# Performance work log

Hardware: AMD Instinct MI355X
Metric: run time of the kernel (lower is better)

The kernel has to match this reference:

```python
import jax, jax.numpy as jnp
import numpy as np

NUM_EMBEDDINGS = 8192
EMBEDDING_DIM = 256
COMMITMENT_COST = 0.25


def setup_inputs() -> dict:
    key = jax.random.key(0)
    k1, k2 = jax.random.split(key)
    z = jax.random.normal(k1, (32, EMBEDDING_DIM, 32, 32), dtype=jnp.float32)
    embedding = jax.random.normal(k2, (EMBEDDING_DIM, NUM_EMBEDDINGS), dtype=jnp.float32)
    return {"z": z, "embedding": embedding}


def reference(z, embedding):
    # z: [B, D, H, W]; embedding: [D, K]
    B, D, H, W = z.shape
    z_perm = jnp.transpose(z, (0, 2, 3, 1))          # [B, H, W, D]
    flat_z = z_perm.reshape(-1, D)                    # [N, D]
    # squared euclidean distances: ||z||^2 - 2 z.e + ||e||^2  -> [N, K]
    distances = (
        jnp.sum(flat_z * flat_z, axis=1, keepdims=True)
        - 2.0 * (flat_z @ embedding)
        + jnp.sum(embedding * embedding, axis=0, keepdims=True)
    )
    encoding_indices = jnp.argmin(distances, axis=1)  # [N]
    # gather codebook rows (same math as one-hot @ embedding.T)
    quantized = jnp.take(embedding.T, encoding_indices, axis=0)  # [N, D]
    quantized = quantized.reshape(z_perm.shape)       # [B, H, W, D]
    quantized = jnp.transpose(quantized, (0, 3, 1, 2))  # [B, D, H, W]

    e_latent_loss = jnp.mean((jax.lax.stop_gradient(quantized) - z) ** 2)
    q_latent_loss = jnp.mean((quantized - jax.lax.stop_gradient(z)) ** 2)
    loss = q_latent_loss + COMMITMENT_COST * e_latent_loss

    # straight-through estimator
    quantized_st = z + jax.lax.stop_gradient(quantized - z)
    return quantized_st, loss
```

## Files before the change

### kernel.cpp

```cpp
#include <hip/hip_runtime.h>

typedef unsigned int u32;
typedef unsigned short u16;
typedef __attribute__((ext_vector_type(8))) short bf16x8;
typedef __attribute__((ext_vector_type(4))) float f32x4;

#define KN 8192
#define DD 256
#define HW 1024
#define NP 32768
#define SPLITS 2
#define KSPLIT 4096
#define BROW 256
#define BCOL 256
#define NTILES (KSPLIT / BCOL)

__device__ __forceinline__ u16 rne_bf16(float x) {
    u32 u = __float_as_uint(x);
    return (u16)((u + 0x7FFF + ((u >> 16) & 1)) >> 16);
}

__device__ __forceinline__ void glds16(const void* g, void* ldsbase) {
    __builtin_amdgcn_global_load_lds((const __attribute__((address_space(1))) u32*)g,
                                     (__attribute__((address_space(3))) u32*)ldsbase, 16, 0, 0);
}

__global__ void prep_kernel(const float* __restrict__ e, const float* __restrict__ z,
                            u16* __restrict__ eT, float* __restrict__ eTf,
                            float* __restrict__ e2f, u16* __restrict__ A) {
    const int t = threadIdx.x;
    const int bid = blockIdx.x;
    if (bid < 32) {
        int k = bid * 256 + t;
        float acc = 0.f;
#pragma unroll 8
        for (int d = 0; d < DD; ++d) {
            float v = e[(size_t)d * KN + k];
            acc = fmaf(v, v, acc);
        }
        e2f[k] = acc;
    } else if (bid < 544) {
        __shared__ float tt[64][65];
        const int b2 = bid - 32;
        const int kt = b2 & 127;
        const int dt = b2 >> 7;
        const float* ep = e + (size_t)(dt * 64) * KN + kt * 64;
        {
            int k = t & 63, d0 = t >> 6;
#pragma unroll
            for (int j = 0; j < 16; ++j) tt[d0 + j * 4][k] = ep[(size_t)(d0 + j * 4) * KN + k];
        }
        __syncthreads();
        int k = t >> 2, c0 = (t & 3) * 16;
        u16 hi[16];
        float fv[16];
#pragma unroll
        for (int j = 0; j < 16; ++j) {
            float v = tt[c0 + j][k];
            fv[j] = v;
            hi[j] = rne_bf16(v);
        }
        u16* rowp = eT + (size_t)(kt * 64 + k) * 256 + dt * 64 + c0;
        *(uint4*)(rowp) = *(uint4*)(hi);
        *(uint4*)(rowp + 8) = *(uint4*)(hi + 8);
        float* rowpf = eTf + (size_t)(kt * 64 + k) * 256 + dt * 64 + c0;
#pragma unroll
        for (int j = 0; j < 4; ++j) *(float4*)(rowpf + j * 4) = *(float4*)(fv + j * 4);
    } else {
        __shared__ float tt[64][65];
        const int b3 = bid - 544;
        const int pt = b3 & 15;
        const int dt = (b3 >> 4) & 3;
        const int b  = b3 >> 6;
        const float* zp = z + (size_t)b * (DD * HW) + (size_t)(dt * 64) * HW + pt * 64;
        {
            int p = t & 63, d0 = t >> 6;
#pragma unroll
            for (int j = 0; j < 16; ++j) tt[d0 + j * 4][p] = zp[(size_t)(d0 + j * 4) * HW + p];
        }
        __syncthreads();
        int p = t >> 2, c0 = (t & 3) * 16;
        int n = b * HW + pt * 64 + p;
        u16 hi[16];
#pragma unroll
        for (int j = 0; j < 16; ++j) hi[j] = rne_bf16(tt[c0 + j][p]);
        u16* rowp = A + (size_t)n * 256 + dt * 64 + c0;
        *(uint4*)(rowp) = *(uint4*)(hi);
        *(uint4*)(rowp + 8) = *(uint4*)(hi + 8);
    }
}


#define STAGE_A(kit)                                                              \
    do {                                                                          \
        const u16* as_ = asrc + (kit) * 32;                                       \
        glds16(as_,             &Ast[(kit) * 8192 + w * 512]);                    \
        glds16(as_ + 128 * 256, &Ast[(kit) * 8192 + (8 + w) * 512]);              \
    } while (0)

#define STAGE_B(eoff, buf)                                                        \
    do {                                                                          \
        const u16* bs_ = bsrc0 + (eoff);                                          \
        glds16(bs_,             &Bst[buf][w * 512]);                              \
        glds16(bs_ + 128 * 256, &Bst[buf][(8 + w) * 512]);                        \
    } while (0)

#define COMPUTE_KIT(kit, first)                                                   \
    do {                                                                          \
        bf16x8 af[4], bfr[8];                                                     \
        const u16* bq_ = &Bst[(kit) & 1][0];                                      \
        _Pragma("unroll")                                                         \
        for (int mi = 0; mi < 4; ++mi)                                            \
            af[mi] = *(const bf16x8*)&Ast[(kit) * 8192 + aoff + mi * 512];        \
        _Pragma("unroll")                                                         \
        for (int ni = 0; ni < 8; ++ni)                                            \
            bfr[ni] = *(const bf16x8*)&bq_[boff + ni * 512];                      \
        __builtin_amdgcn_s_setprio(1);                                            \
        _Pragma("unroll")                                                         \
        for (int mi = 0; mi < 4; ++mi)                                            \
            _Pragma("unroll")                                                     \
            for (int ni = 0; ni < 8; ++ni)                                        \
                acc[mi][ni] = __builtin_amdgcn_mfma_f32_16x16x32_bf16(            \
                    af[mi], bfr[ni], (first) ? zacc : acc[mi][ni], 0, 0, 0);      \
        __builtin_amdgcn_s_setprio(0);                                            \
    } while (0)

__launch_bounds__(512, 2)
__global__ void argmin_mfma_kernel(const u16* __restrict__ A,
                                   const u16* __restrict__ eT,
                                   const float* __restrict__ e2f,
                                   int* __restrict__ keys) {
    __shared__ __align__(16) u16 Ast[8 * 8192];
    __shared__ __align__(16) u16 Bst[2][8192];

    const int t = threadIdx.x;
    const int w = t >> 6;
    const int l = t & 63;
    const int wm = w & 3;
    const int wn = w >> 2;
    const int fr = l & 15;
    const int g  = l >> 4;

    const int split = blockIdx.x & 1;
    const int pxt   = blockIdx.x >> 1;
    const int px0 = pxt * BROW;
    const int kb0 = split * KSPLIT;

    const int srow = l >> 2;
    const int ssw  = ((l & 3) ^ ((l >> 2) & 3)) * 8;
    const u16* asrc  = A  + (size_t)(px0 + w * 16 + srow) * 256 + ssw;
    const u16* bsrc0 = eT + (size_t)(w * 16 + srow) * 256 + ssw;

    const int fsw  = (g ^ (fr & 3)) * 8;
    const int aoff = (wm * 64 + fr) * 32 + fsw;
    const int boff = (wn * 128 + fr) * 32 + fsw;

    const f32x4 zacc = (f32x4){0.f, 0.f, 0.f, 0.f};
    f32x4 acc[4][8];
    int b1[16], b2[16];
#pragma unroll
    for (int i = 0; i < 16; ++i) { b1[i] = 0x7FFFFFFF; b2[i] = 0x7FFFFFFF; }

    auto epilogue = [&](int n0) {
        float e2c[8];
        int   kc8[8];
#pragma unroll
        for (int ni = 0; ni < 8; ++ni) {
            kc8[ni] = n0 + wn * 128 + ni * 16 + fr;
            e2c[ni] = e2f[kc8[ni]] * 256.f;
        }
#pragma unroll
        for (int mi = 0; mi < 4; ++mi)
#pragma unroll
            for (int r = 0; r < 4; ++r) {
                int ky[8];
#pragma unroll
                for (int ni = 0; ni < 8; ++ni) {
                    float d = fmaf(acc[mi][ni][r], -512.f, e2c[ni]);
                    ky[ni] = (int)d * 8192 + kc8[ni];
                }
                int m0 = min(min(ky[0], ky[1]), ky[2]);
                int m1 = min(min(ky[3], ky[4]), ky[5]);
                int m2 = min(min(ky[6], ky[7]), m0);
                int kmin = min(m1, m2);
                int s = mi * 4 + r;
                int v1 = min(b1[s], kmin);
                int x  = max(b1[s], kmin);
                b2[s] = min(b2[s], x);
                b1[s] = v1;
            }
    };

    STAGE_A(0);
    STAGE_B((size_t)kb0 * 256, 0);
    STAGE_A(1);
    asm volatile("s_waitcnt vmcnt(2)" ::: "memory");
    __builtin_amdgcn_s_barrier();

#pragma unroll
    for (int kit = 0; kit < 8; ++kit) {
        if (kit < 7) STAGE_B((size_t)kb0 * 256 + (kit + 1) * 32, (kit + 1) & 1);
        else         STAGE_B(((size_t)kb0 + BCOL) * 256, 0);
        if (kit < 6) STAGE_A(kit + 2);
        COMPUTE_KIT(kit, kit == 0);
        if (kit < 6) { asm volatile("s_waitcnt vmcnt(2)" ::: "memory"); }
        else         { asm volatile("s_waitcnt vmcnt(0)" ::: "memory"); }
        __builtin_amdgcn_s_barrier();
    }
    epilogue(kb0);

    for (int nt = 1; nt < NTILES; ++nt) {
        const int n0 = kb0 + nt * BCOL;
#pragma unroll
        for (int kit = 0; kit < 8; ++kit) {
            if (kit < 7)
                STAGE_B((size_t)n0 * 256 + (kit + 1) * 32, (kit + 1) & 1);
            else if (nt < NTILES - 1)
                STAGE_B(((size_t)n0 + BCOL) * 256, 0);
            COMPUTE_KIT(kit, kit == 0);
            __syncthreads();
        }
        epilogue(n0);
    }

    int* mrg = (int*)&Bst[0][0];
#pragma unroll
    for (int s = 0; s < 16; ++s) {
        int c1 = b1[s], c2 = b2[s], c3 = 0x7FFFFFFF;
#pragma unroll
        for (int m = 1; m < 16; m <<= 1) {
            int a1 = __shfl_xor(c1, m, 64);
            int a2 = __shfl_xor(c2, m, 64);
            int a3 = __shfl_xor(c3, m, 64);
            int m1 = min(c1, a1);
            int xx = max(c1, a1);
            int mn2 = min(c2, a2);
            int m2 = min(xx, mn2);
            int m3 = min(min(max(c2, a2), max(xx, mn2)), min(c3, a3));
            c1 = m1; c2 = m2; c3 = m3;
        }
        if (fr == 0) {
            int row = wm * 64 + (s >> 2) * 16 + g * 4 + (s & 3);
            int o = (wn * 256 + row) * 3;
            mrg[o] = c1; mrg[o + 1] = c2; mrg[o + 2] = c3;
        }
    }
    __syncthreads();
    if (t < 256) {
        int a1 = mrg[t * 3], a2 = mrg[t * 3 + 1], a3 = mrg[t * 3 + 2];
        int u1 = mrg[(256 + t) * 3], u2 = mrg[(256 + t) * 3 + 1], u3 = mrg[(256 + t) * 3 + 2];
        int x1 = min(a1, u1), y1 = max(a1, u1);
        int n2 = min(a2, u2), M2 = max(a2, u2);
        int c1 = x1;
        int c2 = min(y1, n2);
        int c3 = min(max(y1, n2), min(M2, min(a3, u3)));
        int row = px0 + t;
        keys[split * NP + row]       = c1;
        keys[(2 + split) * NP + row] = c2;
        keys[(4 + split) * NP + row] = c3;
    }
}

__global__ void finalize_kernel(const int* __restrict__ keys,
                                const float* __restrict__ z,
                                const float* __restrict__ eTf,
                                const float* __restrict__ e2f,
                                float* __restrict__ out,
                                float* __restrict__ loss) {
    __shared__ float smem[DD * 65];
    __shared__ int   kc[384];
    __shared__ float dval[384];
    __shared__ int   kidx[64];
    const int t = threadIdx.x;
    const int n0 = blockIdx.x * 64;
    const float* zp = z + (size_t)(n0 >> 10) * (DD * HW) + (n0 & (HW - 1));

    for (int i = t; i < DD * 64; i += 256) {
        int d = i >> 6, p = i & 63;
        smem[d * 65 + p] = zp[(size_t)d * HW + p];
    }
    for (int i = t; i < 384; i += 256)
        kc[i] = keys[(i % 6) * NP + n0 + i / 6] & 8191;
    __syncthreads();

    const int l = t & 63, w = t >> 6;
    const int j = l & 15;
    const int s = l >> 4;
#pragma unroll 2
    for (int it = 0; it < 24; ++it) {
        int dot = it * 16 + w * 4 + s;
        int p = dot / 6;
        int k = kc[dot];
        const float* er = eTf + (size_t)k * 256;
        float a = 0.f;
#pragma unroll
        for (int cc = 0; cc < 16; ++cc)
            a = fmaf(smem[(cc * 16 + j) * 65 + p], er[cc * 16 + j], a);
        a += __shfl_xor(a, 1, 64);
        a += __shfl_xor(a, 2, 64);
        a += __shfl_xor(a, 4, 64);
        a += __shfl_xor(a, 8, 64);
        if (j == 0) dval[dot] = fmaf(-2.f, a, e2f[k]);
    }
    __syncthreads();
    if (t < 64) {
        float bv = dval[t * 6];
        int   bk = kc[t * 6];
#pragma unroll
        for (int c = 1; c < 6; ++c) {
            float dv = dval[t * 6 + c];
            int   kk = kc[t * 6 + c];
            if (dv < bv || (dv == bv && kk < bk)) { bv = dv; bk = kk; }
        }
        kidx[t] = bk;
    }
    __syncthreads();

    float* qt = smem;
    for (int m = 0; m < 64; ++m)
        qt[m * 257 + t] = eTf[(size_t)kidx[m] * 256 + t];
    __syncthreads();

    const int p = t & 63, q = t >> 6;
    const size_t base = (size_t)(n0 >> 10) * (DD * HW) + (n0 & (HW - 1)) + p;
    float acc = 0.f;
#pragma unroll 8
    for (int i = 0; i < 64; ++i) {
        int d = q * 64 + i;
        float ev = qt[p * 257 + d];
        float zv = z[base + (size_t)d * HW];
        out[base + (size_t)d * HW] = zv + (ev - zv);
        float df = ev - zv;
        acc = fmaf(df, df, acc);
    }
#pragma unroll
    for (int off = 32; off > 0; off >>= 1) acc += __shfl_down(acc, off, 64);
    __shared__ float part[4];
    if ((t & 63) == 0) part[t >> 6] = acc;
    __syncthreads();
    if (t == 0) {
        float s2 = (part[0] + part[1] + part[2] + part[3]) * (1.25f / 8388608.f);
        atomicAdd(loss, s2);
    }
}

__global__ void combine_kernel(const int* __restrict__ keys,
                               const float* __restrict__ z,
                               const float* __restrict__ eTf,
                               const float* __restrict__ e2f,
                               int* __restrict__ idx) {
    __shared__ float zt[DD * 65];
    __shared__ int   kc[384];
    __shared__ float dval[384];
    const int t = threadIdx.x;
    const int n0 = blockIdx.x * 64;
    const float* zp = z + (size_t)(n0 >> 10) * (DD * HW) + (n0 & (HW - 1));
    for (int i = t; i < DD * 64; i += 256) {
        int d = i >> 6, p = i & 63;
        zt[d * 65 + p] = zp[(size_t)d * HW + p];
    }
    for (int i = t; i < 384; i += 256)
        kc[i] = keys[(i % 6) * NP + n0 + i / 6] & 8191;
    __syncthreads();

    const int l = t & 63, w = t >> 6;
    const int j = l & 15;
    const int s = l >> 4;
#pragma unroll 2
    for (int it = 0; it < 24; ++it) {
        int dot = it * 16 + w * 4 + s;
        int p = dot / 6;
        int k = kc[dot];
        const float* er = eTf + (size_t)k * 256;
        float a = 0.f;
#pragma unroll
        for (int cc = 0; cc < 16; ++cc)
            a = fmaf(zt[(cc * 16 + j) * 65 + p], er[cc * 16 + j], a);
        a += __shfl_xor(a, 1, 64);
        a += __shfl_xor(a, 2, 64);
        a += __shfl_xor(a, 4, 64);
        a += __shfl_xor(a, 8, 64);
        if (j == 0) dval[dot] = fmaf(-2.f, a, e2f[k]);
    }
    __syncthreads();
    if (t < 64) {
        float bv = dval[t * 6];
        int   bk = kc[t * 6];
#pragma unroll
        for (int c = 1; c < 6; ++c) {
            float dv = dval[t * 6 + c];
            int   kk = kc[t * 6 + c];
            if (dv < bv || (dv == bv && kk < bk)) { bv = dv; bk = kk; }
        }
        idx[n0 + t] = bk;
    }
}

__global__ void gather_slow_kernel(const float* __restrict__ z,
                                   const float* __restrict__ e,
                                   const int* __restrict__ idx,
                                   float* __restrict__ out,
                                   float* __restrict__ loss) {
    const int t = threadIdx.x;
    const int n0 = blockIdx.x * 64;
    __shared__ int kidx[64];
    if (t < 64) kidx[t] = idx[n0 + t];
    __syncthreads();

    const int p = t & 63;
    const int d0 = t >> 6;
    const size_t base = (size_t)(n0 >> 10) * (DD * HW) + (n0 & (HW - 1)) + p;
    const int kk = kidx[p];

    float acc = 0.f;
    for (int d = d0; d < DD; d += 4) {
        float ev = e[(size_t)d * KN + kk];
        float zv = z[base + (size_t)d * HW];
        out[base + (size_t)d * HW] = zv + (ev - zv);
        float df = ev - zv;
        acc = fmaf(df, df, acc);
    }
#pragma unroll
    for (int off = 32; off > 0; off >>= 1) acc += __shfl_down(acc, off, 64);
    __shared__ float part[4];
    if ((t & 63) == 0) part[t >> 6] = acc;
    __syncthreads();
    if (t == 0) {
        float s = (part[0] + part[1] + part[2] + part[3]) * (1.25f / 8388608.f);
        atomicAdd(loss, s);
    }
}

extern "C" void kernel_launch(void* const* d_in, const int* in_sizes, int n_in,
                              void* d_out, int out_size, void* d_ws, size_t ws_size,
                              hipStream_t stream) {
    const float* z = (const float*)d_in[0];
    const float* e = (const float*)d_in[1];
    float* out = (float*)d_out;
    float* loss = out + (size_t)NP * DD;

    char* ob = (char*)d_out;
    char* ws = (char*)d_ws;
    u16* Acat = (u16*)ob;
    u16* eT   = (u16*)(ob + ((size_t)16 << 20));

    float* e2f = (float*)ws;
    int*   idx = (int*)(ws + (32 << 10));
    int*   keys;
    float* eTf;
    const bool fastws = ws_size >= ((size_t)10 << 20);
    if (fastws) {
        keys = (int*)(ws + (160 << 10));
        eTf  = (float*)(ws + ((size_t)1 << 20));
    } else {
        keys = (int*)(ob + ((size_t)20 << 20));
        eTf  = (float*)(ob + ((size_t)23 << 20));
    }

    prep_kernel<<<2592, 256, 0, stream>>>(e, z, eT, eTf, e2f, Acat);
    argmin_mfma_kernel<<<SPLITS * (NP / BROW), 512, 0, stream>>>(Acat, eT, e2f, keys);
    hipMemsetAsync(loss, 0, sizeof(float), stream);
    if (fastws) {
        finalize_kernel<<<NP / 64, 256, 0, stream>>>(keys, z, eTf, e2f, out, loss);
    } else {
        combine_kernel<<<NP / 64, 256, 0, stream>>>(keys, z, eTf, e2f, idx);
        gather_slow_kernel<<<NP / 64, 256, 0, stream>>>(z, e, idx, out, loss);
    }
}
```

Baseline: 287.4 us.

## Halve codebook column tile and use 64-wide K chunks with 8-way swizzle

Shrinks the per-block codebook column tile from 256 to 128 and stages 64-element K slices instead of 32, so each wave now computes a 64x64 output with a 4x4 accumulator array. The A tile is loaded in full before the main loop instead of being pipelined through the first tile, and the LDS swizzle moves from 4-way to 8-way XOR over 64-wide rows. The first-tile special case goes away and the distance epilogue is folded into the unified tile loop. The goal is lower register pressure and simpler control flow. The cost is fewer MFMAs per LDS fragment load and a fully exposed A-load latency at the start.

```diff
diff --git a/kernel.cpp b/kernel.cpp
--- a/kernel.cpp
+++ b/kernel.cpp
@@ -12,7 +12,7 @@
 #define SPLITS 2
 #define KSPLIT 4096
 #define BROW 256
-#define BCOL 256
+#define BCOL 128
 #define NTILES (KSPLIT / BCOL)
 
 __device__ __forceinline__ u16 rne_bf16(float x) {
@@ -91,38 +91,37 @@
 }
 
 
-#define STAGE_A(kit)                                                              \
+#define STAGE_B(n0_, kit_, buf_)                                                  \
     do {                                                                          \
-        const u16* as_ = asrc + (kit) * 32;                                       \
-        glds16(as_,             &Ast[(kit) * 8192 + w * 512]);                    \
-        glds16(as_ + 128 * 256, &Ast[(kit) * 8192 + (8 + w) * 512]);              \
+        const u16* bp_ = bsrcw + (size_t)(n0_) * 256 + (kit_) * 64;               \
+        glds16(bp_,           &Bd[buf_][(w * 16) * 64]);                          \
+        glds16(bp_ + 8 * 256, &Bd[buf_][(w * 16 + 8) * 64]);                      \
     } while (0)
 
-#define STAGE_B(eoff, buf)                                                        \
+#define COMPUTE_KIT(kit_, cur_, first_)                                           \
     do {                                                                          \
-        const u16* bs_ = bsrc0 + (eoff);                                          \
-        glds16(bs_,             &Bst[buf][w * 512]);                              \
-        glds16(bs_ + 128 * 256, &Bst[buf][(8 + w) * 512]);                        \
-    } while (0)
-
-#define COMPUTE_KIT(kit, first)                                                   \
-    do {                                                                          \
-        bf16x8 af[4], bfr[8];                                                     \
-        const u16* bq_ = &Bst[(kit) & 1][0];                                      \
         _Pragma("unroll")                                                         \
-        for (int mi = 0; mi < 4; ++mi)                                            \
-            af[mi] = *(const bf16x8*)&Ast[(kit) * 8192 + aoff + mi * 512];        \
-        _Pragma("unroll")                                                         \
-        for (int ni = 0; ni < 8; ++ni)                                            \
-            bfr[ni] = *(const bf16x8*)&bq_[boff + ni * 512];                      \
-        __builtin_amdgcn_s_setprio(1);                                            \
-        _Pragma("unroll")                                                         \
-        for (int mi = 0; mi < 4; ++mi)                                            \
+        for (int kc = 0; kc < 2; ++kc) {                                          \
+            const int sl_ = ((kc * 4 + g) ^ (fr & 7)) * 8;                        \
+            const int ao_ = (wm * 64 + fr) * 64 + sl_;                            \
+            const int bo_ = (wn * 64 + fr) * 64 + sl_;                            \
+            bf16x8 af[4], bfr[4];                                                 \
             _Pragma("unroll")                                                     \
-            for (int ni = 0; ni < 8; ++ni)                                        \
-                acc[mi][ni] = __builtin_amdgcn_mfma_f32_16x16x32_bf16(            \
-                    af[mi], bfr[ni], (first) ? zacc : acc[mi][ni], 0, 0, 0);      \
-        __builtin_amdgcn_s_setprio(0);                                            \
+            for (int mi = 0; mi < 4; ++mi)                                        \
+                af[mi] = *(const bf16x8*)&Ast[kit_][ao_ + mi * 1024];             \
+            _Pragma("unroll")                                                     \
+            for (int ni = 0; ni < 4; ++ni)                                        \
+                bfr[ni] = *(const bf16x8*)&Bd[cur_][bo_ + ni * 1024];             \
+            __builtin_amdgcn_s_setprio(1);                                        \
+            _Pragma("unroll")                                                     \
+            for (int mi = 0; mi < 4; ++mi)                                        \
+                _Pragma("unroll")                                                 \
+                for (int ni = 0; ni < 4; ++ni)                                    \
+                    acc[mi][ni] = __builtin_amdgcn_mfma_f32_16x16x32_bf16(        \
+                        af[mi], bfr[ni],                                          \
+                        ((first_) && kc == 0) ? zacc : acc[mi][ni], 0, 0, 0);     \
+            __builtin_amdgcn_s_setprio(0);                                        \
+        }                                                                         \
     } while (0)
 
 __launch_bounds__(512, 2)
@@ -130,8 +129,8 @@
                                    const u16* __restrict__ eT,
                                    const float* __restrict__ e2f,
                                    int* __restrict__ keys) {
-    __shared__ __align__(16) u16 Ast[8 * 8192];
-    __shared__ __align__(16) u16 Bst[2][8192];
+    __shared__ __align__(16) u16 Ast[4][BROW * 64];
+    __shared__ __align__(16) u16 Bd[2][BCOL * 64];
 
     const int t = threadIdx.x;
     const int w = t >> 6;
@@ -146,84 +145,64 @@
     const int px0 = pxt * BROW;
     const int kb0 = split * KSPLIT;
 
-    const int srow = l >> 2;
-    const int ssw  = ((l & 3) ^ ((l >> 2) & 3)) * 8;
-    const u16* asrc  = A  + (size_t)(px0 + w * 16 + srow) * 256 + ssw;
-    const u16* bsrc0 = eT + (size_t)(w * 16 + srow) * 256 + ssw;
-
-    const int fsw  = (g ^ (fr & 3)) * 8;
-    const int aoff = (wm * 64 + fr) * 32 + fsw;
-    const int boff = (wn * 128 + fr) * 32 + fsw;
+    const int srow = l >> 3;
+    const int ssw  = ((l & 7) ^ srow) * 8;
+    const u16* asrc  = A  + (size_t)(px0 + w * 32 + srow) * 256 + ssw;
+    const u16* bsrcw = eT + (size_t)(w * 16 + srow) * 256 + ssw;
 
     const f32x4 zacc = (f32x4){0.f, 0.f, 0.f, 0.f};
-    f32x4 acc[4][8];
+    f32x4 acc[4][4];
     int b1[16], b2[16];
 #pragma unroll
     for (int i = 0; i < 16; ++i) { b1[i] = 0x7FFFFFFF; b2[i] = 0x7FFFFFFF; }
 
-    auto epilogue = [&](int n0) {
-        float e2c[8];
-        int   kc8[8];
-#pragma unroll
-        for (int ni = 0; ni < 8; ++ni) {
-            kc8[ni] = n0 + wn * 128 + ni * 16 + fr;
-            e2c[ni] = e2f[kc8[ni]] * 256.f;
+    STAGE_B(kb0, 0, 0);
+#pragma unroll
+    for (int kit = 0; kit < 4; ++kit)
+#pragma unroll
+        for (int i = 0; i < 4; ++i)
+            glds16(asrc + kit * 64 + (size_t)(i * 8) * 256,
+                   &Ast[kit][(w * 32 + i * 8) * 64]);
+    __syncthreads();
+
+    for (int nt = 0; nt < NTILES; ++nt) {
+        const int n0 = kb0 + nt * BCOL;
+#pragma unroll
+        for (int kit = 0; kit < 4; ++kit) {
+            const int cur = kit & 1;
+            if (kit < 3)               STAGE_B(n0, kit + 1, cur ^ 1);
+            else if (nt < NTILES - 1)  STAGE_B(n0 + BCOL, 0, cur ^ 1);
+            COMPUTE_KIT(kit, cur, kit == 0);
+            __syncthreads();
+        }
+
+        float e2c[4];
+        int   kc4[4];
+#pragma unroll
+        for (int ni = 0; ni < 4; ++ni) {
+            kc4[ni] = n0 + wn * 64 + ni * 16 + fr;
+            e2c[ni] = e2f[kc4[ni]] * 256.f;
         }
 #pragma unroll
         for (int mi = 0; mi < 4; ++mi)
 #pragma unroll
             for (int r = 0; r < 4; ++r) {
-                int ky[8];
-#pragma unroll
-                for (int ni = 0; ni < 8; ++ni) {
+                int ky[4];
+#pragma unroll
+                for (int ni = 0; ni < 4; ++ni) {
                     float d = fmaf(acc[mi][ni][r], -512.f, e2c[ni]);
-                    ky[ni] = (int)d * 8192 + kc8[ni];
+                    ky[ni] = (int)d * 8192 + kc4[ni];
                 }
-                int m0 = min(min(ky[0], ky[1]), ky[2]);
-                int m1 = min(min(ky[3], ky[4]), ky[5]);
-                int m2 = min(min(ky[6], ky[7]), m0);
-                int kmin = min(m1, m2);
+                int kmin = min(min(ky[0], ky[1]), min(ky[2], ky[3]));
                 int s = mi * 4 + r;
                 int v1 = min(b1[s], kmin);
                 int x  = max(b1[s], kmin);
                 b2[s] = min(b2[s], x);
                 b1[s] = v1;
             }
-    };
-
-    STAGE_A(0);
-    STAGE_B((size_t)kb0 * 256, 0);
-    STAGE_A(1);
-    asm volatile("s_waitcnt vmcnt(2)" ::: "memory");
-    __builtin_amdgcn_s_barrier();
-
-#pragma unroll
-    for (int kit = 0; kit < 8; ++kit) {
-        if (kit < 7) STAGE_B((size_t)kb0 * 256 + (kit + 1) * 32, (kit + 1) & 1);
-        else         STAGE_B(((size_t)kb0 + BCOL) * 256, 0);
-        if (kit < 6) STAGE_A(kit + 2);
-        COMPUTE_KIT(kit, kit == 0);
-        if (kit < 6) { asm volatile("s_waitcnt vmcnt(2)" ::: "memory"); }
-        else         { asm volatile("s_waitcnt vmcnt(0)" ::: "memory"); }
-        __builtin_amdgcn_s_barrier();
-    }
-    epilogue(kb0);
-
-    for (int nt = 1; nt < NTILES; ++nt) {
-        const int n0 = kb0 + nt * BCOL;
-#pragma unroll
-        for (int kit = 0; kit < 8; ++kit) {
-            if (kit < 7)
-                STAGE_B((size_t)n0 * 256 + (kit + 1) * 32, (kit + 1) & 1);
-            else if (nt < NTILES - 1)
-                STAGE_B(((size_t)n0 + BCOL) * 256, 0);
-            COMPUTE_KIT(kit, kit == 0);
-            __syncthreads();
-        }
-        epilogue(n0);
-    }
-
-    int* mrg = (int*)&Bst[0][0];
+    }
+
+    int* mrg = (int*)&Bd[0][0];
 #pragma unroll
     for (int s = 0; s < 16; ++s) {
         int c1 = b1[s], c2 = b2[s], c3 = 0x7FFFFFFF;
```

Measured after the change: 298.0 us. 1.04x slower.
